# Optimization experiments

Hardware: AMD Instinct MI355X
Metric: run time of the kernel (lower is better)

The kernel has to match this reference:

```python
import jax, jax.numpy as jnp
import numpy as np

N = 50000      # nodes
E = 800000     # edges (avg degree 16)
IN = 512       # in_feats
HID = 64       # hidden_dim
HEADS = 4      # num_heads
NC = 40        # num_classes


def setup_inputs() -> dict:
    key = jax.random.key(0)
    ks = jax.random.split(key, 12)

    def p(k, shape, fan_in):
        return jax.random.normal(k, shape, jnp.float32) * (1.0 / np.sqrt(fan_in))

    x = jax.random.normal(ks[0], (N, IN), jnp.float32)
    edge_index = jax.random.randint(ks[1], (2, E), 0, N)
    return dict(
        x=x,
        edge_index=edge_index,
        W1=p(ks[2], (IN, HEADS * HID), IN),
        att_src1=p(ks[3], (HEADS, HID), HID),
        att_dst1=p(ks[4], (HEADS, HID), HID),
        b1=jnp.zeros((HEADS * HID,), jnp.float32),
        W2=p(ks[5], (HEADS * HID, HID), HEADS * HID),
        att_src2=p(ks[6], (1, HID), HID),
        att_dst2=p(ks[7], (1, HID), HID),
        b2=jnp.zeros((HID,), jnp.float32),
        mw1=p(ks[8], (HID, 64), HID),
        mb1=jnp.zeros((64,), jnp.float32),
        mw2=p(ks[9], (64, NC), 64),
        mb2=jnp.zeros((NC,), jnp.float32),
    )


def gat_layer(x, edge_index, W, att_src, att_dst, bias):
    # PyG GATConv with add_self_loops=False, concat=True, negative_slope=0.2
    H, C = att_src.shape
    n = x.shape[0]
    h = (x @ W).reshape(n, H, C)                       # [N,H,C]
    a_src = jnp.sum(h * att_src, axis=-1)              # [N,H]
    a_dst = jnp.sum(h * att_dst, axis=-1)              # [N,H]
    src, dst = edge_index[0], edge_index[1]
    e = jax.nn.leaky_relu(a_src[src] + a_dst[dst], 0.2)  # [E,H]
    # segment softmax grouped by destination node
    m = jax.ops.segment_max(e, dst, num_segments=n)
    ex = jnp.exp(e - m[dst])
    denom = jax.ops.segment_sum(ex, dst, num_segments=n)
    alpha = ex / (denom[dst] + 1e-16)                  # [E,H]
    out = jax.ops.segment_sum(h[src] * alpha[:, :, None], dst, num_segments=n)  # [N,H,C]
    return out.reshape(n, H * C) + bias


def reference(x, edge_index, W1, att_src1, att_dst1, b1,
              W2, att_src2, att_dst2, b2, mw1, mb1, mw2, mb2):
    h = jax.nn.elu(gat_layer(x, edge_index, W1, att_src1, att_dst1, b1))   # [N, HEADS*HID]
    emb = gat_layer(h, edge_index, W2, att_src2, att_dst2, b2)             # [N, HID] (heads=1)
    return jax.nn.relu(emb @ mw1 + mb1) @ mw2 + mb2                        # [N, NC]
```

## Files before the change

kernel.cpp:

```cpp
#include <hip/hip_runtime.h>

#define N_NODES 50000
#define N_EDGES 800000
#define SCAN_B 196

typedef short bf16x8 __attribute__((ext_vector_type(8)));
typedef short bf16x4 __attribute__((ext_vector_type(4)));
typedef float f32x4 __attribute__((ext_vector_type(4)));

#define GLDS16(g, l)                                                  \
  __builtin_amdgcn_global_load_lds(                                   \
      (const __attribute__((address_space(1))) void*)(g),             \
      (__attribute__((address_space(3))) void*)(l), 16, 0, 0)

__device__ __forceinline__ unsigned short f2bf_rne(float x) {
  unsigned u = __float_as_uint(x);
  u += 0x7FFFu + ((u >> 16) & 1u);
  return (unsigned short)(u >> 16);
}

__device__ __forceinline__ void split2(float x, short& hi, short& lo) {
  unsigned u = __float_as_uint(x);
  unsigned short h = (unsigned short)(u >> 16);
  float hf = __uint_as_float((unsigned)h << 16);
  float r = x - hf;
  unsigned short l = (unsigned short)(__float_as_uint(r) >> 16);
  hi = (short)h;
  lo = (short)l;
}

__global__ __launch_bounds__(256) void hist_k(const int* __restrict__ ei,
                                              int* __restrict__ cnt) {
  int e = blockIdx.x * 256 + threadIdx.x;
  if (e >= N_EDGES) return;
  atomicAdd(&cnt[ei[N_EDGES + e]], 1);
}

__global__ __launch_bounds__(256) void scan1(const int* __restrict__ cnt,
                                             int* __restrict__ offs,
                                             int* __restrict__ bsum) {
  __shared__ int sh[256];
  int t = threadIdx.x;
  int i = blockIdx.x * 256 + t;
  int v = (i < N_NODES) ? cnt[i] : 0;
  sh[t] = v;
  __syncthreads();
  for (int off = 1; off < 256; off <<= 1) {
    int add = (t >= off) ? sh[t - off] : 0;
    __syncthreads();
    sh[t] += add;
    __syncthreads();
  }
  if (i < N_NODES) offs[i] = sh[t] - v;
  if (t == 255) bsum[blockIdx.x] = sh[255];
}

__global__ __launch_bounds__(256) void scan2(const int* __restrict__ bsum,
                                             int* __restrict__ bofs) {
  __shared__ int sh[256];
  int t = threadIdx.x;
  int v = (t < SCAN_B) ? bsum[t] : 0;
  sh[t] = v;
  __syncthreads();
  for (int off = 1; off < 256; off <<= 1) {
    int add = (t >= off) ? sh[t - off] : 0;
    __syncthreads();
    sh[t] += add;
    __syncthreads();
  }
  if (t < SCAN_B) bofs[t] = sh[t] - v;
}

__global__ __launch_bounds__(256) void scan3(int* __restrict__ offs,
                                             const int* __restrict__ bofs) {
  int i = blockIdx.x * 256 + threadIdx.x;
  if (i < N_NODES) offs[i] += bofs[blockIdx.x];
  if (i == 0) offs[N_NODES] = N_EDGES;
}

__global__ __launch_bounds__(256) void scatter_k(const int* __restrict__ ei,
                                                 const int* __restrict__ offs,
                                                 int* __restrict__ cur,
                                                 int* __restrict__ ssort) {
  int e = blockIdx.x * 256 + threadIdx.x;
  if (e >= N_EDGES) return;
  int d = ei[N_EDGES + e];
  int p = offs[d] + atomicAdd(&cur[d], 1);
  ssort[p] = ei[e];
}

__global__ __launch_bounds__(256) void wsplit(
    const float* __restrict__ W, unsigned short* __restrict__ Wh,
    unsigned short* __restrict__ Wl, int K, int Nn) {
  int i = blockIdx.x * 256 + threadIdx.x;
  int total = (K >> 3) * Nn;
  if (i >= total) return;
  int kq = i / Nn;
  int n = i % Nn;
  alignas(16) short h[8], l[8];
#pragma unroll
  for (int j = 0; j < 8; ++j) {
    float v = W[(size_t)(kq * 8 + j) * Nn + n];
    split2(v, h[j], l[j]);
  }
  size_t dst = (size_t)i * 8;
  *(bf16x8*)&Wh[dst] = *(bf16x8*)h;
  *(bf16x8*)&Wl[dst] = *(bf16x8*)l;
}

__global__ __launch_bounds__(256) void gemm1_fused(
    const float* __restrict__ A,
    const unsigned short* __restrict__ Bh_g, const unsigned short* __restrict__ Bl_g,
    const float* __restrict__ att_s, const float* __restrict__ att_d,
    unsigned short* __restrict__ h1b, float* __restrict__ asrc,
    float* __restrict__ adst, int M) {
  constexpr int K = 512, Nn = 256;
  constexpr int LDA = 40;
  __shared__ short Ah[128][LDA], Al[128][LDA];
  __shared__ short Bh[4 * 128 * 8], Bl[4 * 128 * 8];
  __shared__ float attLds[128][4];

  const int tid = threadIdx.x;
  const int wave = tid >> 6, lane = tid & 63;
  const int quad = lane >> 4, l16 = lane & 15;
  const int wm = (wave >> 1) * 64, wn = (wave & 1) * 64;
  const int rowBase = blockIdx.x * 128;
  const int colBase = blockIdx.y * 128;

  const int ra = tid >> 1, apart = (tid & 1) * 16;
  const int arow = min(rowBase + ra, M - 1);
  const float* aptr = A + (size_t)arow * K + apart;

  f32x4 acc[4][4] = {};

  for (int kc = 0; kc < K / 32; ++kc) {
#pragma unroll
    for (int inst = 0; inst < 2; ++inst) {
      int seq = inst * 256 + tid;
      int gq = seq >> 7, nl = seq & 127;
      size_t gsrc = (((size_t)kc * 4 + gq) * Nn + colBase + nl) * 8;
      GLDS16(Bh_g + gsrc, &Bh[seq * 8]);
      GLDS16(Bl_g + gsrc, &Bl[seq * 8]);
    }
    {
      alignas(16) short h[16], l[16];
      const float4* a4 = (const float4*)(aptr + kc * 32);
#pragma unroll
      for (int i = 0; i < 4; ++i) {
        float4 v = a4[i];
        split2(v.x, h[i * 4 + 0], l[i * 4 + 0]);
        split2(v.y, h[i * 4 + 1], l[i * 4 + 1]);
        split2(v.z, h[i * 4 + 2], l[i * 4 + 2]);
        split2(v.w, h[i * 4 + 3], l[i * 4 + 3]);
      }
      *(bf16x8*)&Ah[ra][apart]     = ((bf16x8*)h)[0];
      *(bf16x8*)&Ah[ra][apart + 8] = ((bf16x8*)h)[1];
      *(bf16x8*)&Al[ra][apart]     = ((bf16x8*)l)[0];
      *(bf16x8*)&Al[ra][apart + 8] = ((bf16x8*)l)[1];
    }
    __syncthreads();
    bf16x8 afh[4], afl[4], bfh[4], bfl[4];
#pragma unroll
    for (int mt = 0; mt < 4; ++mt) {
      afh[mt] = *(const bf16x8*)&Ah[wm + mt * 16 + l16][quad * 8];
      afl[mt] = *(const bf16x8*)&Al[wm + mt * 16 + l16][quad * 8];
    }
#pragma unroll
    for (int nt = 0; nt < 4; ++nt) {
      int bi = ((quad << 7) + wn + nt * 16 + l16) * 8;
      bfh[nt] = *(const bf16x8*)&Bh[bi];
      bfl[nt] = *(const bf16x8*)&Bl[bi];
    }
#pragma unroll
    for (int mt = 0; mt < 4; ++mt)
#pragma unroll
      for (int nt = 0; nt < 4; ++nt) {
        acc[mt][nt] = __builtin_amdgcn_mfma_f32_16x16x32_bf16(afh[mt], bfh[nt], acc[mt][nt], 0, 0, 0);
        acc[mt][nt] = __builtin_amdgcn_mfma_f32_16x16x32_bf16(afh[mt], bfl[nt], acc[mt][nt], 0, 0, 0);
        acc[mt][nt] = __builtin_amdgcn_mfma_f32_16x16x32_bf16(afl[mt], bfh[nt], acc[mt][nt], 0, 0, 0);
      }
    __syncthreads();
  }

  float asw[4], adw[4];
#pragma unroll
  for (int nt = 0; nt < 4; ++nt) {
    int c = colBase + wn + nt * 16 + l16;
    asw[nt] = att_s[c];
    adw[nt] = att_d[c];
  }
#pragma unroll
  for (int mt = 0; mt < 4; ++mt) {
    int rl = wm + mt * 16 + quad * 4;
#pragma unroll
    for (int reg = 0; reg < 4; ++reg) {
      int r = rowBase + rl + reg;
      float s = 0.f, dd = 0.f;
#pragma unroll
      for (int nt = 0; nt < 4; ++nt) {
        float v = acc[mt][nt][reg];
        s += v * asw[nt];
        dd += v * adw[nt];
        if (r < M) {
          int c = colBase + wn + nt * 16 + l16;
          h1b[(size_t)r * Nn + c] = f2bf_rne(v);
        }
      }
#pragma unroll
      for (int off = 1; off < 16; off <<= 1) {
        s += __shfl_xor(s, off);
        dd += __shfl_xor(dd, off);
      }
      if (l16 == 0) {
        attLds[rl + reg][(wn >> 6) * 2 + 0] = s;
        attLds[rl + reg][(wn >> 6) * 2 + 1] = dd;
      }
    }
  }
  __syncthreads();
  if (tid < 128) {
    int r = rowBase + tid;
    if (r < M) {
      int hb = colBase >> 6;
      asrc[r * 4 + hb + 0] = attLds[tid][0];
      adst[r * 4 + hb + 0] = attLds[tid][1];
      asrc[r * 4 + hb + 1] = attLds[tid][2];
      adst[r * 4 + hb + 1] = attLds[tid][3];
    }
  }
}

__global__ __launch_bounds__(256) void gemm2_fused(
    const float* __restrict__ A,
    const unsigned short* __restrict__ Bh_g, const unsigned short* __restrict__ Bl_g,
    const float* __restrict__ att_s, const float* __restrict__ att_d,
    unsigned short* __restrict__ h2b, float* __restrict__ asrc,
    float* __restrict__ adst, int M) {
  constexpr int K = 256, Nn = 64;
  constexpr int LDA = 40;
  __shared__ short Ah[128][LDA], Al[128][LDA];
  __shared__ short Bh[4 * 64 * 8], Bl[4 * 64 * 8];
  __shared__ float attLds[128][2];

  const int tid = threadIdx.x;
  const int wave = tid >> 6, lane = tid & 63;
  const int quad = lane >> 4, l16 = lane & 15;
  const int wm = wave * 32;
  const int rowBase = blockIdx.x * 128;

  const int ra = tid >> 1, apart = (tid & 1) * 16;
  const int arow = min(rowBase + ra, M - 1);
  const float* aptr = A + (size_t)arow * K + apart;

  f32x4 acc[2][4] = {};

  for (int kc = 0; kc < K / 32; ++kc) {
    {
      size_t gsrc = (((size_t)kc * 4) * Nn) * 8 + (size_t)tid * 8;
      GLDS16(Bh_g + gsrc, &Bh[tid * 8]);
      GLDS16(Bl_g + gsrc, &Bl[tid * 8]);
    }
    {
      alignas(16) short h[16], l[16];
      const float4* a4 = (const float4*)(aptr + kc * 32);
#pragma unroll
      for (int i = 0; i < 4; ++i) {
        float4 v = a4[i];
        split2(v.x, h[i * 4 + 0], l[i * 4 + 0]);
        split2(v.y, h[i * 4 + 1], l[i * 4 + 1]);
        split2(v.z, h[i * 4 + 2], l[i * 4 + 2]);
        split2(v.w, h[i * 4 + 3], l[i * 4 + 3]);
      }
      *(bf16x8*)&Ah[ra][apart]     = ((bf16x8*)h)[0];
      *(bf16x8*)&Ah[ra][apart + 8] = ((bf16x8*)h)[1];
      *(bf16x8*)&Al[ra][apart]     = ((bf16x8*)l)[0];
      *(bf16x8*)&Al[ra][apart + 8] = ((bf16x8*)l)[1];
    }
    __syncthreads();
    bf16x8 afh[2], afl[2], bfh[4], bfl[4];
#pragma unroll
    for (int mt = 0; mt < 2; ++mt) {
      afh[mt] = *(const bf16x8*)&Ah[wm + mt * 16 + l16][quad * 8];
      afl[mt] = *(const bf16x8*)&Al[wm + mt * 16 + l16][quad * 8];
    }
#pragma unroll
    for (int nt = 0; nt < 4; ++nt) {
      int bi = ((quad << 6) + nt * 16 + l16) * 8;
      bfh[nt] = *(const bf16x8*)&Bh[bi];
      bfl[nt] = *(const bf16x8*)&Bl[bi];
    }
#pragma unroll
    for (int mt = 0; mt < 2; ++mt)
#pragma unroll
      for (int nt = 0; nt < 4; ++nt) {
        acc[mt][nt] = __builtin_amdgcn_mfma_f32_16x16x32_bf16(afh[mt], bfh[nt], acc[mt][nt], 0, 0, 0);
        acc[mt][nt] = __builtin_amdgcn_mfma_f32_16x16x32_bf16(afh[mt], bfl[nt], acc[mt][nt], 0, 0, 0);
        acc[mt][nt] = __builtin_amdgcn_mfma_f32_16x16x32_bf16(afl[mt], bfh[nt], acc[mt][nt], 0, 0, 0);
      }
    __syncthreads();
  }

  float asw[4], adw[4];
#pragma unroll
  for (int nt = 0; nt < 4; ++nt) {
    int c = nt * 16 + l16;
    asw[nt] = att_s[c];
    adw[nt] = att_d[c];
  }
#pragma unroll
  for (int mt = 0; mt < 2; ++mt) {
    int rl = wm + mt * 16 + quad * 4;
#pragma unroll
    for (int reg = 0; reg < 4; ++reg) {
      int r = rowBase + rl + reg;
      float s = 0.f, dd = 0.f;
#pragma unroll
      for (int nt = 0; nt < 4; ++nt) {
        float v = acc[mt][nt][reg];
        s += v * asw[nt];
        dd += v * adw[nt];
        if (r < M) {
          int c = nt * 16 + l16;
          h2b[(size_t)r * Nn + c] = f2bf_rne(v);
        }
      }
#pragma unroll
      for (int off = 1; off < 16; off <<= 1) {
        s += __shfl_xor(s, off);
        dd += __shfl_xor(dd, off);
      }
      if (l16 == 0) {
        attLds[rl + reg][0] = s;
        attLds[rl + reg][1] = dd;
      }
    }
  }
  __syncthreads();
  if (tid < 128) {
    int r = rowBase + tid;
    if (r < M) {
      asrc[r] = attLds[tid][0];
      adst[r] = attLds[tid][1];
    }
  }
}

__global__ __launch_bounds__(128) void agg_l1(
    const int* __restrict__ offs, const int* __restrict__ ssort,
    const float* __restrict__ asrc, const float* __restrict__ adst,
    const unsigned short* __restrict__ h1b, const float* __restrict__ b1,
    float* __restrict__ outp) {
  const int d = blockIdx.x;
  const int t = threadIdx.x;
  const int g = t >> 5, lt = t & 31;
  const int h = lt >> 3;
  __shared__ int s_src[32];
  __shared__ float s_ex[32 * 4];
  __shared__ float red[4][32][9];
  const int row0 = offs[d], row1 = offs[d + 1];
  const float4 ad4 = *(const float4*)&adst[d * 4];
  float acc[8] = {};
  float denom = 0.f;

  for (int j0 = row0; j0 < row1; j0 += 32) {
    const int n = min(32, row1 - j0);
    if (t < n) {
      int s = ssort[j0 + t];
      s_src[t] = s;
      float4 as = *(const float4*)&asrc[s * 4];
      float4 sc;
      sc.x = as.x + ad4.x; sc.x = sc.x > 0.f ? sc.x : 0.2f * sc.x;
      sc.y = as.y + ad4.y; sc.y = sc.y > 0.f ? sc.y : 0.2f * sc.y;
      sc.z = as.z + ad4.z; sc.z = sc.z > 0.f ? sc.z : 0.2f * sc.z;
      sc.w = as.w + ad4.w; sc.w = sc.w > 0.f ? sc.w : 0.2f * sc.w;
      sc.x = __expf(sc.x); sc.y = __expf(sc.y);
      sc.z = __expf(sc.z); sc.w = __expf(sc.w);
      *(float4*)&s_ex[t * 4] = sc;
    }
    __syncthreads();
    for (int jj = g; jj < n; jj += 4) {
      int s = s_src[jj];
      float exv = s_ex[jj * 4 + h];
      bf16x8 pv = *(const bf16x8*)&h1b[(size_t)s * 256 + lt * 8];
#pragma unroll
      for (int k = 0; k < 8; ++k) {
        float f = __uint_as_float((unsigned)(unsigned short)pv[k] << 16);
        acc[k] += f * exv;
      }
      denom += exv;
    }
    __syncthreads();
  }
#pragma unroll
  for (int k = 0; k < 8; ++k) red[g][lt][k] = acc[k];
  red[g][lt][8] = denom;
  __syncthreads();
  if (g == 0) {
    float a[8], dn;
    dn = red[0][lt][8] + red[1][lt][8] + red[2][lt][8] + red[3][lt][8];
#pragma unroll
    for (int k = 0; k < 8; ++k)
      a[k] = red[0][lt][k] + red[1][lt][k] + red[2][lt][k] + red[3][lt][k];
    float inv = dn > 0.f ? 1.f / dn : 0.f;
    float o[8];
#pragma unroll
    for (int k = 0; k < 8; ++k) {
      float v = a[k] * inv + b1[lt * 8 + k];
      o[k] = v > 0.f ? v : expm1f(v);
    }
    float4 r0 = {o[0], o[1], o[2], o[3]};
    float4 r1 = {o[4], o[5], o[6], o[7]};
    *(float4*)&outp[(size_t)d * 256 + lt * 8]     = r0;
    *(float4*)&outp[(size_t)d * 256 + lt * 8 + 4] = r1;
  }
}

__global__ __launch_bounds__(256) void agg_l2(
    const int* __restrict__ offs, const int* __restrict__ ssort,
    const float* __restrict__ asrc, const float* __restrict__ adst,
    const unsigned short* __restrict__ h2b, const float* __restrict__ b2,
    float* __restrict__ outp, int n_nodes) {
  int d = blockIdx.x * 4 + (threadIdx.x >> 6);
  int lane = threadIdx.x & 63;
  if (d >= n_nodes) return;
  const int eg = lane >> 4, fl = lane & 15;
  const int row0 = offs[d], row1 = offs[d + 1];
  const float ad = adst[d];
  float acc[4] = {};
  float denom = 0.f;

  for (int j0 = row0; j0 < row1; j0 += 4) {
    int jm = j0 + eg;
    int s = 0;
    float ex = 0.f;
    if (jm < row1) {
      s = ssort[jm];
      float sc = asrc[s] + ad;
      sc = sc > 0.f ? sc : 0.2f * sc;
      ex = __expf(sc);
    }
    bf16x4 pv = *(const bf16x4*)&h2b[(size_t)s * 64 + fl * 4];
#pragma unroll
    for (int k = 0; k < 4; ++k) {
      float f = __uint_as_float((unsigned)(unsigned short)pv[k] << 16);
      acc[k] += f * ex;
    }
    denom += ex;
  }
#pragma unroll
  for (int k = 0; k < 4; ++k) {
    acc[k] += __shfl_xor(acc[k], 16);
    acc[k] += __shfl_xor(acc[k], 32);
  }
  denom += __shfl_xor(denom, 16);
  denom += __shfl_xor(denom, 32);
  float inv = denom > 0.f ? 1.f / denom : 0.f;
  if (eg == 0) {
    float4 r;
    r.x = acc[0] * inv + b2[fl * 4 + 0];
    r.y = acc[1] * inv + b2[fl * 4 + 1];
    r.z = acc[2] * inv + b2[fl * 4 + 2];
    r.w = acc[3] * inv + b2[fl * 4 + 3];
    *(float4*)&outp[(size_t)d * 64 + fl * 4] = r;
  }
}

__global__ __launch_bounds__(256) void mlp_head(
    const float* __restrict__ emb_in,
    const float* __restrict__ mw1, const float* __restrict__ mb1,
    const float* __restrict__ mw2, const float* __restrict__ mb2,
    float* __restrict__ outp, int n) {
  __shared__ float w1s[64 * 64];
  __shared__ float w2s[64 * 40];
  __shared__ float b1s[64];
  __shared__ float b2s[40];
  int t = threadIdx.x;
  for (int i = t; i < 64 * 64; i += 256) w1s[i] = mw1[i];
  for (int i = t; i < 64 * 40; i += 256) w2s[i] = mw2[i];
  if (t < 64) b1s[t] = mb1[t];
  if (t < 40) b2s[t] = mb2[t];
  __syncthreads();
  int node = blockIdx.x * 256 + t;
  if (node >= n) return;
  float emb[64];
#pragma unroll
  for (int i = 0; i < 64; ++i) emb[i] = emb_in[(size_t)node * 64 + i];
  float hid[64];
#pragma unroll
  for (int j = 0; j < 64; ++j) {
    float s = b1s[j];
#pragma unroll
    for (int i = 0; i < 64; ++i) s += emb[i] * w1s[i * 64 + j];
    hid[j] = s > 0.f ? s : 0.f;
  }
#pragma unroll
  for (int k = 0; k < 40; ++k) {
    float s = b2s[k];
#pragma unroll
    for (int j = 0; j < 64; ++j) s += hid[j] * w2s[j * 40 + k];
    outp[(size_t)node * 40 + k] = s;
  }
}

extern "C" void kernel_launch(void* const* d_in, const int* in_sizes, int n_in,
                              void* d_out, int out_size, void* d_ws, size_t ws_size,
                              hipStream_t stream) {
  const float* x        = (const float*)d_in[0];
  const int*   ei       = (const int*)d_in[1];
  const float* W1       = (const float*)d_in[2];
  const float* att_src1 = (const float*)d_in[3];
  const float* att_dst1 = (const float*)d_in[4];
  const float* b1       = (const float*)d_in[5];
  const float* W2       = (const float*)d_in[6];
  const float* att_src2 = (const float*)d_in[7];
  const float* att_dst2 = (const float*)d_in[8];
  const float* b2       = (const float*)d_in[9];
  const float* mw1      = (const float*)d_in[10];
  const float* mb1      = (const float*)d_in[11];
  const float* mw2      = (const float*)d_in[12];
  const float* mb2      = (const float*)d_in[13];
  float* out = (float*)d_out;

  const int N = N_NODES, E = N_EDGES;
  char* base = (char*)d_ws;
  size_t o = 0;
  auto alloc = [&](size_t n_elems) {
    void* p = base + o;
    o = (o + n_elems * 4 + 15) & ~(size_t)15;
    return p;
  };
  int* cnt = (int*)alloc(N);
  int* cur = (int*)alloc(N);
  size_t zero_bytes = o;
  int*   offs  = (int*)alloc(N + 2);
  int*   bsum  = (int*)alloc(256);
  int*   bofs  = (int*)alloc(256);
  int*   ssort = (int*)alloc(E);
  float* h1e   = (float*)alloc((size_t)N * 256);
  float* asrc1 = (float*)alloc((size_t)N * 4);
  float* adst1 = (float*)alloc((size_t)N * 4);
  float* emb   = (float*)alloc((size_t)N * 64);
  float* asrc2 = (float*)alloc(N);
  float* adst2 = (float*)alloc(N);
  unsigned short* h1b = (unsigned short*)alloc((size_t)N * 128);
  unsigned short* h2b = (unsigned short*)alloc((size_t)N * 32);
  unsigned short* w1h = (unsigned short*)alloc(512 * 256 / 2);
  unsigned short* w1l = (unsigned short*)alloc(512 * 256 / 2);
  unsigned short* w2h = (unsigned short*)alloc(256 * 64 / 2);
  unsigned short* w2l = (unsigned short*)alloc(256 * 64 / 2);

  hipMemsetAsync(d_ws, 0, zero_bytes, stream);

  const int EB = (E + 255) / 256;

  hist_k<<<EB, 256, 0, stream>>>(ei, cnt);
  scan1<<<SCAN_B, 256, 0, stream>>>(cnt, offs, bsum);
  scan2<<<1, 256, 0, stream>>>(bsum, bofs);
  scan3<<<SCAN_B, 256, 0, stream>>>(offs, bofs);
  scatter_k<<<EB, 256, 0, stream>>>(ei, offs, cur, ssort);
  wsplit<<<(512 / 8 * 256 + 255) / 256, 256, 0, stream>>>(W1, w1h, w1l, 512, 256);
  wsplit<<<(256 / 8 * 64 + 255) / 256, 256, 0, stream>>>(W2, w2h, w2l, 256, 64);

  dim3 g1((N + 127) / 128, 2);
  gemm1_fused<<<g1, 256, 0, stream>>>(x, w1h, w1l, att_src1, att_dst1,
                                      h1b, asrc1, adst1, N);
  agg_l1<<<N, 128, 0, stream>>>(offs, ssort, asrc1, adst1, h1b, b1, h1e);

  dim3 g2((N + 127) / 128, 1);
  gemm2_fused<<<g2, 256, 0, stream>>>(h1e, w2h, w2l, att_src2, att_dst2,
                                      h2b, asrc2, adst2, N);
  agg_l2<<<(N + 3) / 4, 256, 0, stream>>>(offs, ssort, asrc2, adst2, h2b, b2, emb, N);

  mlp_head<<<(N + 255) / 256, 256, 0, stream>>>(emb, mw1, mb1, mw2, mb2, out, N);
}
```

Baseline: 516.5 us.

## Assign one node per 32-lane group in aggregations with register prefetch pipeline

Rewrites both aggregation kernels so that each destination node is handled by a sub-wave group (32 lanes for layer 1, 16 lanes for layer 2). Each group walks its edges serially and software-prefetches the next source row and attention score. This removes the shared-memory staging, block barriers and cross-group reductions, and packs many nodes into one block instead of launching one block per node. It also merges the two weight-split launches into one. In exchange, per-edge parallelism within a node drops, so high-degree nodes run longer and latency hiding relies on the one-ahead prefetch.

```diff
diff --git a/kernel.cpp b/kernel.cpp
--- a/kernel.cpp
+++ b/kernel.cpp
@@ -89,21 +89,31 @@
   ssort[p] = ei[e];
 }
 
-__global__ __launch_bounds__(256) void wsplit(
-    const float* __restrict__ W, unsigned short* __restrict__ Wh,
-    unsigned short* __restrict__ Wl, int K, int Nn) {
+__global__ __launch_bounds__(256) void wsplit_all(
+    const float* __restrict__ W1, unsigned short* __restrict__ W1h,
+    unsigned short* __restrict__ W1l,
+    const float* __restrict__ W2, unsigned short* __restrict__ W2h,
+    unsigned short* __restrict__ W2l) {
   int i = blockIdx.x * 256 + threadIdx.x;
-  int total = (K >> 3) * Nn;
-  if (i >= total) return;
-  int kq = i / Nn;
-  int n = i % Nn;
+  const float* W;
+  unsigned short *Wh, *Wl;
+  int Nn, c;
+  if (i < 16384) {
+    W = W1; Wh = W1h; Wl = W1l; Nn = 256; c = i;
+  } else if (i < 16384 + 2048) {
+    W = W2; Wh = W2h; Wl = W2l; Nn = 64; c = i - 16384;
+  } else {
+    return;
+  }
+  int kq = c / Nn;
+  int n = c % Nn;
   alignas(16) short h[8], l[8];
 #pragma unroll
   for (int j = 0; j < 8; ++j) {
     float v = W[(size_t)(kq * 8 + j) * Nn + n];
     split2(v, h[j], l[j]);
   }
-  size_t dst = (size_t)i * 8;
+  size_t dst = (size_t)c * 8;
   *(bf16x8*)&Wh[dst] = *(bf16x8*)h;
   *(bf16x8*)&Wl[dst] = *(bf16x8*)l;
 }
@@ -345,74 +355,58 @@
   }
 }
 
-__global__ __launch_bounds__(128) void agg_l1(
+__global__ __launch_bounds__(256) void agg_l1(
     const int* __restrict__ offs, const int* __restrict__ ssort,
     const float* __restrict__ asrc, const float* __restrict__ adst,
     const unsigned short* __restrict__ h1b, const float* __restrict__ b1,
-    float* __restrict__ outp) {
-  const int d = blockIdx.x;
+    float* __restrict__ outp, int n_nodes) {
   const int t = threadIdx.x;
   const int g = t >> 5, lt = t & 31;
+  const int d = blockIdx.x * 8 + g;
+  if (d >= n_nodes) return;
   const int h = lt >> 3;
-  __shared__ int s_src[32];
-  __shared__ float s_ex[32 * 4];
-  __shared__ float red[4][32][9];
   const int row0 = offs[d], row1 = offs[d + 1];
-  const float4 ad4 = *(const float4*)&adst[d * 4];
+  const float ad = adst[d * 4 + h];
   float acc[8] = {};
   float denom = 0.f;
 
-  for (int j0 = row0; j0 < row1; j0 += 32) {
-    const int n = min(32, row1 - j0);
-    if (t < n) {
-      int s = ssort[j0 + t];
-      s_src[t] = s;
-      float4 as = *(const float4*)&asrc[s * 4];
-      float4 sc;
-      sc.x = as.x + ad4.x; sc.x = sc.x > 0.f ? sc.x : 0.2f * sc.x;
-      sc.y = as.y + ad4.y; sc.y = sc.y > 0.f ? sc.y : 0.2f * sc.y;
-      sc.z = as.z + ad4.z; sc.z = sc.z > 0.f ? sc.z : 0.2f * sc.z;
-      sc.w = as.w + ad4.w; sc.w = sc.w > 0.f ? sc.w : 0.2f * sc.w;
-      sc.x = __expf(sc.x); sc.y = __expf(sc.y);
-      sc.z = __expf(sc.z); sc.w = __expf(sc.w);
-      *(float4*)&s_ex[t * 4] = sc;
-    }
-    __syncthreads();
-    for (int jj = g; jj < n; jj += 4) {
-      int s = s_src[jj];
-      float exv = s_ex[jj * 4 + h];
-      bf16x8 pv = *(const bf16x8*)&h1b[(size_t)s * 256 + lt * 8];
+  if (row0 < row1) {
+    int s_cur = ssort[row0];
+    float a_cur = asrc[s_cur * 4 + h];
+    bf16x8 p_cur = *(const bf16x8*)&h1b[(size_t)s_cur * 256 + lt * 8];
+    int s_next = (row0 + 1 < row1) ? ssort[row0 + 1] : s_cur;
+    for (int j = row0; j < row1; ++j) {
+      float a_nxt = 0.f;
+      bf16x8 p_nxt = {};
+      int s_n2 = s_next;
+      if (j + 1 < row1) {
+        a_nxt = asrc[s_next * 4 + h];
+        p_nxt = *(const bf16x8*)&h1b[(size_t)s_next * 256 + lt * 8];
+        s_n2 = (j + 2 < row1) ? ssort[j + 2] : s_next;
+      }
+      float sc = a_cur + ad;
+      sc = sc > 0.f ? sc : 0.2f * sc;
+      float ex = __expf(sc);
 #pragma unroll
       for (int k = 0; k < 8; ++k) {
-        float f = __uint_as_float((unsigned)(unsigned short)pv[k] << 16);
-        acc[k] += f * exv;
-      }
-      denom += exv;
-    }
-    __syncthreads();
-  }
-#pragma unroll
-  for (int k = 0; k < 8; ++k) red[g][lt][k] = acc[k];
-  red[g][lt][8] = denom;
-  __syncthreads();
-  if (g == 0) {
-    float a[8], dn;
-    dn = red[0][lt][8] + red[1][lt][8] + red[2][lt][8] + red[3][lt][8];
-#pragma unroll
-    for (int k = 0; k < 8; ++k)
-      a[k] = red[0][lt][k] + red[1][lt][k] + red[2][lt][k] + red[3][lt][k];
-    float inv = dn > 0.f ? 1.f / dn : 0.f;
-    float o[8];
-#pragma unroll
-    for (int k = 0; k < 8; ++k) {
-      float v = a[k] * inv + b1[lt * 8 + k];
-      o[k] = v > 0.f ? v : expm1f(v);
-    }
-    float4 r0 = {o[0], o[1], o[2], o[3]};
-    float4 r1 = {o[4], o[5], o[6], o[7]};
-    *(float4*)&outp[(size_t)d * 256 + lt * 8]     = r0;
-    *(float4*)&outp[(size_t)d * 256 + lt * 8 + 4] = r1;
-  }
+        float f = __uint_as_float((unsigned)(unsigned short)p_cur[k] << 16);
+        acc[k] += f * ex;
+      }
+      denom += ex;
+      a_cur = a_nxt;
+      p_cur = p_nxt;
+      s_next = s_n2;
+    }
+  }
+  float inv = denom > 0.f ? 1.f / denom : 0.f;
+  float o[8];
+#pragma unroll
+  for (int k = 0; k < 8; ++k) {
+    float v = acc[k] * inv + b1[lt * 8 + k];
+    o[k] = v > 0.f ? v : expm1f(v);
+  }
+  *(float4*)&outp[(size_t)d * 256 + lt * 8]     = *(float4*)&o[0];
+  *(float4*)&outp[(size_t)d * 256 + lt * 8 + 4] = *(float4*)&o[4];
 }
 
 __global__ __launch_bounds__(256) void agg_l2(
@@ -420,49 +414,50 @@
     const float* __restrict__ asrc, const float* __restrict__ adst,
     const unsigned short* __restrict__ h2b, const float* __restrict__ b2,
     float* __restrict__ outp, int n_nodes) {
-  int d = blockIdx.x * 4 + (threadIdx.x >> 6);
-  int lane = threadIdx.x & 63;
+  const int t = threadIdx.x;
+  const int g = t >> 4, lt = t & 15;
+  const int d = blockIdx.x * 16 + g;
   if (d >= n_nodes) return;
-  const int eg = lane >> 4, fl = lane & 15;
   const int row0 = offs[d], row1 = offs[d + 1];
   const float ad = adst[d];
   float acc[4] = {};
   float denom = 0.f;
 
-  for (int j0 = row0; j0 < row1; j0 += 4) {
-    int jm = j0 + eg;
-    int s = 0;
-    float ex = 0.f;
-    if (jm < row1) {
-      s = ssort[jm];
-      float sc = asrc[s] + ad;
+  if (row0 < row1) {
+    int s_cur = ssort[row0];
+    float a_cur = asrc[s_cur];
+    bf16x4 p_cur = *(const bf16x4*)&h2b[(size_t)s_cur * 64 + lt * 4];
+    int s_next = (row0 + 1 < row1) ? ssort[row0 + 1] : s_cur;
+    for (int j = row0; j < row1; ++j) {
+      float a_nxt = 0.f;
+      bf16x4 p_nxt = {};
+      int s_n2 = s_next;
+      if (j + 1 < row1) {
+        a_nxt = asrc[s_next];
+        p_nxt = *(const bf16x4*)&h2b[(size_t)s_next * 64 + lt * 4];
+        s_n2 = (j + 2 < row1) ? ssort[j + 2] : s_next;
+      }
+      float sc = a_cur + ad;
       sc = sc > 0.f ? sc : 0.2f * sc;
-      ex = __expf(sc);
-    }
-    bf16x4 pv = *(const bf16x4*)&h2b[(size_t)s * 64 + fl * 4];
-#pragma unroll
-    for (int k = 0; k < 4; ++k) {
-      float f = __uint_as_float((unsigned)(unsigned short)pv[k] << 16);
-      acc[k] += f * ex;
-    }
-    denom += ex;
-  }
-#pragma unroll
-  for (int k = 0; k < 4; ++k) {
-    acc[k] += __shfl_xor(acc[k], 16);
-    acc[k] += __shfl_xor(acc[k], 32);
-  }
-  denom += __shfl_xor(denom, 16);
-  denom += __shfl_xor(denom, 32);
+      float ex = __expf(sc);
+#pragma unroll
+      for (int k = 0; k < 4; ++k) {
+        float f = __uint_as_float((unsigned)(unsigned short)p_cur[k] << 16);
+        acc[k] += f * ex;
+      }
+      denom += ex;
+      a_cur = a_nxt;
+      p_cur = p_nxt;
+      s_next = s_n2;
+    }
+  }
   float inv = denom > 0.f ? 1.f / denom : 0.f;
-  if (eg == 0) {
-    float4 r;
-    r.x = acc[0] * inv + b2[fl * 4 + 0];
-    r.y = acc[1] * inv + b2[fl * 4 + 1];
-    r.z = acc[2] * inv + b2[fl * 4 + 2];
-    r.w = acc[3] * inv + b2[fl * 4 + 3];
-    *(float4*)&outp[(size_t)d * 64 + fl * 4] = r;
-  }
+  float4 r;
+  r.x = acc[0] * inv + b2[lt * 4 + 0];
+  r.y = acc[1] * inv + b2[lt * 4 + 1];
+  r.z = acc[2] * inv + b2[lt * 4 + 2];
+  r.w = acc[3] * inv + b2[lt * 4 + 3];
+  *(float4*)&outp[(size_t)d * 64 + lt * 4] = r;
 }
 
 __global__ __launch_bounds__(256) void mlp_head(
@@ -558,18 +553,20 @@
   scan2<<<1, 256, 0, stream>>>(bsum, bofs);
   scan3<<<SCAN_B, 256, 0, stream>>>(offs, bofs);
   scatter_k<<<EB, 256, 0, stream>>>(ei, offs, cur, ssort);
-  wsplit<<<(512 / 8 * 256 + 255) / 256, 256, 0, stream>>>(W1, w1h, w1l, 512, 256);
-  wsplit<<<(256 / 8 * 64 + 255) / 256, 256, 0, stream>>>(W2, w2h, w2l, 256, 64);
+  wsplit_all<<<(16384 + 2048 + 255) / 256, 256, 0, stream>>>(W1, w1h, w1l,
+                                                             W2, w2h, w2l);
 
   dim3 g1((N + 127) / 128, 2);
   gemm1_fused<<<g1, 256, 0, stream>>>(x, w1h, w1l, att_src1, att_dst1,
                                       h1b, asrc1, adst1, N);
-  agg_l1<<<N, 128, 0, stream>>>(offs, ssort, asrc1, adst1, h1b, b1, h1e);
+  agg_l1<<<(N + 7) / 8, 256, 0, stream>>>(offs, ssort, asrc1, adst1, h1b, b1,
+                                          h1e, N);
 
   dim3 g2((N + 127) / 128, 1);
   gemm2_fused<<<g2, 256, 0, stream>>>(h1e, w2h, w2l, att_src2, att_dst2,
                                       h2b, asrc2, adst2, N);
-  agg_l2<<<(N + 3) / 4, 256, 0, stream>>>(offs, ssort, asrc2, adst2, h2b, b2, emb, N);
+  agg_l2<<<(N + 15) / 16, 256, 0, stream>>>(offs, ssort, asrc2, adst2, h2b, b2,
+                                            emb, N);
 
   mlp_head<<<(N + 255) / 256, 256, 0, stream>>>(emb, mw1, mb1, mw2, mb2, out, N);
 }
```

After: 492.6 us. -4.6%, faster.
